# Optimization experiments

Hardware: AMD Instinct MI355X
Metric: run time of the kernel (lower is better)

The kernel has to match this reference:

```python
import jax, jax.numpy as jnp
import numpy as np

ATTN_SIZE = 64
ENC_SIZE = 512
HIDDEN_SIZE = 512
L, B = 2048, 64


def setup_inputs() -> dict:
    key = jax.random.key(0)
    k1, k2, k3, k4, k5, k6 = jax.random.split(key, 6)
    enc_outputs = jax.random.normal(k1, (L, B, ENC_SIZE), dtype=jnp.float32)
    lens = jax.random.randint(k2, (B,), 1, L + 1, dtype=jnp.int32)
    hidden_states = jax.random.normal(k3, (B, HIDDEN_SIZE), dtype=jnp.float32)
    # Xavier-normal params as in reset_params()
    W_enc = jax.random.normal(k4, (ENC_SIZE, ATTN_SIZE), dtype=jnp.float32) * np.sqrt(2.0 / (ENC_SIZE + ATTN_SIZE))
    W_hidden = jax.random.normal(k5, (HIDDEN_SIZE, ATTN_SIZE), dtype=jnp.float32) * np.sqrt(2.0 / (HIDDEN_SIZE + ATTN_SIZE))
    b_attn = jnp.zeros((ATTN_SIZE,), dtype=jnp.float32)
    v = jax.random.normal(k6, (ATTN_SIZE,), dtype=jnp.float32)
    return {"enc_outputs": enc_outputs, "lens": lens, "hidden_states": hidden_states,
            "W_enc": W_enc, "b_attn": b_attn, "W_hidden": W_hidden, "v": v}


def reference(enc_outputs, lens, hidden_states, W_enc, b_attn, W_hidden, v):
    l = enc_outputs.shape[0]
    # parts: (l, b, attn_size) — projection of encoder outputs
    parts = jnp.einsum('lbd,da->lba', enc_outputs, W_enc) + b_attn
    # additive (Bahdanau) score: tanh(parts + h @ W_hidden) . v -> (l, b)
    hid = hidden_states @ W_hidden  # (b, attn_size)
    scores = jnp.sum(jnp.tanh(parts + hid[None, :, :]) * v, axis=2)
    # faithful mask: 1.0 at valid positions, -inf at padding (original adds 1, a
    # constant shift that softmax cancels, but we reproduce the exact math)
    valid = jnp.arange(l, dtype=lens.dtype)[:, None] < lens[None, :]  # (l, b)
    mask = jnp.where(valid, jnp.float32(1.0), -jnp.inf)
    w = jax.nn.softmax(scores + mask, axis=0)  # softmax over sequence dim
    # weighted sum over sequence: (b, d)
    return jnp.einsum('lb,lbd->bd', w, enc_outputs)
```

## Files before the change

### kernel.cpp

```cpp
#include <hip/hip_runtime.h>
#include <hip/hip_bf16.h>
#include <math.h>

#define L_DIM 2048
#define B_DIM 64
#define D_DIM 512
#define A_DIM 64

#define SUB_L 16
#define CHUNK_L 64
#define N_SUB (CHUNK_L / SUB_L)
#define N_CHUNK (L_DIM / CHUNK_L)
#define EPAD 520

typedef __attribute__((ext_vector_type(8))) short bf16x8;
typedef __attribute__((ext_vector_type(4))) float f32x4;

__device__ __forceinline__ void split_bf16(float x, short& hi, short& lo) {
    __hip_bfloat16 h = __float2bfloat16(x);
    float hf = __bfloat162float(h);
    __hip_bfloat16 l = __float2bfloat16(x - hf);
    hi = *reinterpret_cast<short*>(&h);
    lo = *reinterpret_cast<short*>(&l);
}

__device__ __forceinline__ void split_pair(float x, float y,
                                           unsigned& hi2, unsigned& lo2) {
    unsigned ux = __float_as_uint(x), uy = __float_as_uint(y);
    hi2 = __builtin_amdgcn_perm(uy, ux, 0x07060302u);
    float rx = x - __uint_as_float(ux & 0xFFFF0000u);
    float ry = y - __uint_as_float(uy & 0xFFFF0000u);
    lo2 = __builtin_amdgcn_perm(__float_as_uint(ry), __float_as_uint(rx),
                                0x07060302u);
}

__device__ __forceinline__ float bf_hi_lo(short h, short l) {
    unsigned uh = ((unsigned)(unsigned short)h) << 16;
    unsigned ul = ((unsigned)(unsigned short)l) << 16;
    return __uint_as_float(uh) + __uint_as_float(ul);
}

__device__ __forceinline__ float fast_tanh(float x) {
    float e = __expf(2.0f * x);
    return 1.0f - 2.0f / (e + 1.0f);
}

__device__ __forceinline__ void lds_barrier() {
    asm volatile("s_waitcnt lgkmcnt(0)" ::: "memory");
    __builtin_amdgcn_s_barrier();
}

__global__ __launch_bounds__(256) void setup_kernel(
    const float* __restrict__ hidden, const float* __restrict__ Wh,
    const float* __restrict__ battn, const float* __restrict__ We,
    float* __restrict__ hb, short* __restrict__ wt_hi,
    short* __restrict__ wt_lo) {
    __shared__ float part[4][A_DIM];
    if (blockIdx.x < 64) {
        const int b = blockIdx.x;
        const int a = threadIdx.x & 63;
        const int sl = threadIdx.x >> 6;
        const float* hrow = hidden + b * D_DIM + sl * 128;
        const float* wcol = Wh + (size_t)sl * 128 * A_DIM + a;
        float acc = 0.f;
#pragma unroll 8
        for (int d = 0; d < 128; ++d) acc += hrow[d] * wcol[(size_t)d * A_DIM];
        part[sl][a] = acc;
        __syncthreads();
        if (sl == 0)
            hb[b * A_DIM + a] =
                battn[a] + part[0][a] + part[1][a] + part[2][a] + part[3][a];
    } else {
        const int base = (blockIdx.x - 64) * 1024 + threadIdx.x * 4;
#pragma unroll
        for (int t = 0; t < 4; ++t) {
            const int i = base + t;
            const int a = i & 63;
            const int d = i >> 6;
            short h, l;
            split_bf16(We[i], h, l);
            wt_hi[a * D_DIM + d] = h;
            wt_lo[a * D_DIM + d] = l;
        }
    }
}

__global__ __launch_bounds__(256, 2) void fused_kernel(
    const float* __restrict__ enc, const short* __restrict__ wt_hi,
    const short* __restrict__ wt_lo, const float* __restrict__ hb,
    const float* __restrict__ v, const int* __restrict__ lens,
    float* __restrict__ Om, float* __restrict__ mz) {
    const int c = blockIdx.x;
    const int b = blockIdx.y;
    const int tid = threadIdx.x;
    const int wave = tid >> 6;
    const int lane = tid & 63;
    const int quad = lane >> 4;
    const int l15 = lane & 15;
    const int po = tid & 127;
    const int par = tid >> 7;

    __shared__ short Ehi[2][SUB_L][EPAD];
    __shared__ short Elo[2][SUB_L][EPAD];
    __shared__ float sred[SUB_L][4];
    __shared__ float ored[D_DIM];

    const int len_b = lens[b];
    const int a_col = wave * 16 + l15;
    const float hb0 = hb[b * A_DIM + a_col];
    const float v0 = v[a_col];

    const short* bh = wt_hi + (size_t)a_col * D_DIM + quad * 8;
    const short* bl = wt_lo + (size_t)a_col * D_DIM + quad * 8;
    bf16x8 Bh[16], Bl[16];
#pragma unroll
    for (int s = 0; s < 16; ++s) {
        Bh[s] = *(const bf16x8*)(bh + s * 32);
        Bl[s] = *(const bf16x8*)(bl + s * 32);
    }

    float4 Oacc = {0.f, 0.f, 0.f, 0.f};
    float mA = -INFINITY, ZA = 0.f;

    const float* encb = enc + (size_t)c * CHUNK_L * B_DIM * D_DIM +
                        (size_t)b * D_DIM + po * 4;
    const size_t ROWSTRIDE = (size_t)B_DIM * D_DIM;

    float4 buf[8];
#pragma unroll
    for (int j = 0; j < 8; ++j)
        buf[j] = *(const float4*)(encb + (size_t)(2 * j + par) * ROWSTRIDE);

#pragma unroll 2
    for (int sub = 0; sub < N_SUB; ++sub) {
        const int cb = sub & 1;

#pragma unroll
        for (int j = 0; j < 8; ++j) {
            const int li = 2 * j + par;
            uint2 h2, l2;
            split_pair(buf[j].x, buf[j].y, h2.x, l2.x);
            split_pair(buf[j].z, buf[j].w, h2.y, l2.y);
            *(uint2*)&Ehi[cb][li][po * 4] = h2;
            *(uint2*)&Elo[cb][li][po * 4] = l2;
        }
        lds_barrier();

        if (sub + 1 < N_SUB) {
            const float* p = encb + (size_t)(sub + 1) * SUB_L * ROWSTRIDE;
#pragma unroll
            for (int j = 0; j < 8; ++j)
                buf[j] = *(const float4*)(p + (size_t)(2 * j + par) * ROWSTRIDE);
        }

        f32x4 a0 = {0.f, 0.f, 0.f, 0.f};
        f32x4 a1 = {0.f, 0.f, 0.f, 0.f};
        f32x4 a2 = {0.f, 0.f, 0.f, 0.f};
#pragma unroll
        for (int s = 0; s < 16; ++s) {
            const int k = s * 32;
            const bf16x8 Ah = *(const bf16x8*)&Ehi[cb][l15][k + quad * 8];
            const bf16x8 Al = *(const bf16x8*)&Elo[cb][l15][k + quad * 8];
            a0 = __builtin_amdgcn_mfma_f32_16x16x32_bf16(Ah, Bh[s], a0, 0, 0, 0);
            a1 = __builtin_amdgcn_mfma_f32_16x16x32_bf16(Ah, Bl[s], a1, 0, 0, 0);
            a2 = __builtin_amdgcn_mfma_f32_16x16x32_bf16(Al, Bh[s], a2, 0, 0, 0);
        }

#pragma unroll
        for (int r = 0; r < 4; ++r) {
            float t = fast_tanh(a0[r] + a1[r] + a2[r] + hb0) * v0;
            t += __shfl_xor(t, 1);
            t += __shfl_xor(t, 2);
            t += __shfl_xor(t, 4);
            t += __shfl_xor(t, 8);
            if (l15 == 0) sred[quad * 4 + r][wave] = t;
        }
        lds_barrier();

        float s = sred[l15][0] + sred[l15][1] + sred[l15][2] + sred[l15][3];
        const int lg = c * CHUNK_L + sub * SUB_L + l15;
        s = (lg < len_b) ? (s + 1.0f) : -INFINITY;
        float m = s;
        m = fmaxf(m, __shfl_xor(m, 1));
        m = fmaxf(m, __shfl_xor(m, 2));
        m = fmaxf(m, __shfl_xor(m, 4));
        m = fmaxf(m, __shfl_xor(m, 8));
        const float w = (m == -INFINITY) ? 0.f : __expf(s - m);
        float z = w;
        z += __shfl_xor(z, 1);
        z += __shfl_xor(z, 2);
        z += __shfl_xor(z, 4);
        z += __shfl_xor(z, 8);

        const float mN = fmaxf(mA, m);
        const float cA = (mA == -INFINITY) ? 0.f : __expf(mA - mN);
        const float cS = (m == -INFINITY) ? 0.f : __expf(m - mN);
        Oacc.x *= cA; Oacc.y *= cA; Oacc.z *= cA; Oacc.w *= cA;
#pragma unroll
        for (int j = 0; j < 8; ++j) {
            const int li = 2 * j + par;
            const float wgt = cS * __shfl(w, li);
            const short4 h4 = *(const short4*)&Ehi[cb][li][po * 4];
            const short4 l4 = *(const short4*)&Elo[cb][li][po * 4];
            Oacc.x += wgt * bf_hi_lo(h4.x, l4.x);
            Oacc.y += wgt * bf_hi_lo(h4.y, l4.y);
            Oacc.z += wgt * bf_hi_lo(h4.z, l4.z);
            Oacc.w += wgt * bf_hi_lo(h4.w, l4.w);
        }
        ZA = cA * ZA + cS * z;
        mA = mN;
    }

    if (par == 0) *(float4*)&ored[po * 4] = Oacc;
    __syncthreads();
    if (par == 1) {
        const float4 o0 = *(const float4*)&ored[po * 4];
        float4 r;
        r.x = o0.x + Oacc.x;
        r.y = o0.y + Oacc.y;
        r.z = o0.z + Oacc.z;
        r.w = o0.w + Oacc.w;
        *(float4*)(Om + ((size_t)b * N_CHUNK + c) * D_DIM + po * 4) = r;
    }
    if (tid == 0) {
        mz[((size_t)b * N_CHUNK + c) * 2 + 0] = mA;
        mz[((size_t)b * N_CHUNK + c) * 2 + 1] = ZA;
    }
}

__global__ __launch_bounds__(256) void combine_kernel(
    const float* __restrict__ Om, const float* __restrict__ mz,
    float* __restrict__ out) {
    const int b = blockIdx.x;
    const int tid = threadIdx.x;
    __shared__ float coef[N_CHUNK];
    __shared__ float sinv;

    if (tid < 32) {
        const float m = mz[((size_t)b * N_CHUNK + tid) * 2 + 0];
        const float Z = mz[((size_t)b * N_CHUNK + tid) * 2 + 1];
        float mm = m;
        mm = fmaxf(mm, __shfl_xor(mm, 1));
        mm = fmaxf(mm, __shfl_xor(mm, 2));
        mm = fmaxf(mm, __shfl_xor(mm, 4));
        mm = fmaxf(mm, __shfl_xor(mm, 8));
        mm = fmaxf(mm, __shfl_xor(mm, 16));
        const float cc = (m == -INFINITY) ? 0.f : __expf(m - mm);
        coef[tid] = cc;
        float s = cc * Z;
        s += __shfl_xor(s, 1);
        s += __shfl_xor(s, 2);
        s += __shfl_xor(s, 4);
        s += __shfl_xor(s, 8);
        s += __shfl_xor(s, 16);
        if (tid == 0) sinv = 1.0f / s;
    }
    __syncthreads();

    const float* base = Om + (size_t)b * N_CHUNK * D_DIM + tid * 2;
    float ox = 0.f, oy = 0.f;
#pragma unroll 8
    for (int cc = 0; cc < N_CHUNK; ++cc) {
        const float2 x = *(const float2*)(base + cc * D_DIM);
        ox += coef[cc] * x.x;
        oy += coef[cc] * x.y;
    }
    const float s = sinv;
    *(float2*)(out + (size_t)b * D_DIM + tid * 2) = make_float2(ox * s, oy * s);
}

extern "C" void kernel_launch(void* const* d_in, const int* in_sizes, int n_in,
                              void* d_out, int out_size, void* d_ws, size_t ws_size,
                              hipStream_t stream) {
    const float* enc    = (const float*)d_in[0];
    const int*   lens   = (const int*)d_in[1];
    const float* hidden = (const float*)d_in[2];
    const float* We     = (const float*)d_in[3];
    const float* battn  = (const float*)d_in[4];
    const float* Wh     = (const float*)d_in[5];
    const float* v      = (const float*)d_in[6];
    float* out = (float*)d_out;

    char* w8 = (char*)d_ws;
    float* hb    = (float*)(w8 + 0);
    short* wt_hi = (short*)(w8 + 16 * 1024);
    short* wt_lo = (short*)(w8 + 80 * 1024);
    float* mz    = (float*)(w8 + 144 * 1024);
    float* Om    = (float*)(w8 + 160 * 1024);

    setup_kernel<<<96, 256, 0, stream>>>(hidden, Wh, battn, We, hb, wt_hi, wt_lo);
    fused_kernel<<<dim3(N_CHUNK, B_DIM), 256, 0, stream>>>(
        enc, wt_hi, wt_lo, hb, v, lens, Om, mz);
    combine_kernel<<<B_DIM, 256, 0, stream>>>(Om, mz, out);
}
```

Baseline: 419.1 us.

## Single-buffer LDS, transpose MFMA operands, and simplify score reduction for higher occupancy

Drops the double-buffered E tiles to a single buffer and adds a trailing barrier so the LDS footprint shrinks, then raises launch bounds to allow three blocks per CU. Swaps MFMA operand order so each lane holds four attention columns of one row. The tanh·v reduction then needs only two cross-lane shuffles instead of sixteen. Every thread now recomputes the 16-row max and sum from shared memory, which removes the shuffle-based broadcast of weights. The risks are register spills under the tighter occupancy bound and the extra barrier per sub-tile.

Result: slower. 522.2 us (+24.6%).

```diff
diff --git a/kernel.cpp b/kernel.cpp
--- a/kernel.cpp
+++ b/kernel.cpp
@@ -85,7 +85,7 @@
     }
 }
 
-__global__ __launch_bounds__(256, 2) void fused_kernel(
+__global__ __launch_bounds__(256, 3) void fused_kernel(
     const float* __restrict__ enc, const short* __restrict__ wt_hi,
     const short* __restrict__ wt_lo, const float* __restrict__ hb,
     const float* __restrict__ v, const int* __restrict__ lens,
@@ -100,15 +100,15 @@
     const int po = tid & 127;
     const int par = tid >> 7;
 
-    __shared__ short Ehi[2][SUB_L][EPAD];
-    __shared__ short Elo[2][SUB_L][EPAD];
-    __shared__ float sred[SUB_L][4];
+    __shared__ short Ehi[SUB_L][EPAD];
+    __shared__ short Elo[SUB_L][EPAD];
+    __shared__ __align__(16) float sred[SUB_L][4];
     __shared__ float ored[D_DIM];
 
     const int len_b = lens[b];
     const int a_col = wave * 16 + l15;
-    const float hb0 = hb[b * A_DIM + a_col];
-    const float v0 = v[a_col];
+    const float4 hb4 = *(const float4*)(hb + b * A_DIM + wave * 16 + quad * 4);
+    const float4 v4  = *(const float4*)(v + wave * 16 + quad * 4);
 
     const short* bh = wt_hi + (size_t)a_col * D_DIM + quad * 8;
     const short* bl = wt_lo + (size_t)a_col * D_DIM + quad * 8;
@@ -131,18 +131,16 @@
     for (int j = 0; j < 8; ++j)
         buf[j] = *(const float4*)(encb + (size_t)(2 * j + par) * ROWSTRIDE);
 
-#pragma unroll 2
+#pragma unroll 1
     for (int sub = 0; sub < N_SUB; ++sub) {
-        const int cb = sub & 1;
-
 #pragma unroll
         for (int j = 0; j < 8; ++j) {
             const int li = 2 * j + par;
             uint2 h2, l2;
             split_pair(buf[j].x, buf[j].y, h2.x, l2.x);
             split_pair(buf[j].z, buf[j].w, h2.y, l2.y);
-            *(uint2*)&Ehi[cb][li][po * 4] = h2;
-            *(uint2*)&Elo[cb][li][po * 4] = l2;
+            *(uint2*)&Ehi[li][po * 4] = h2;
+            *(uint2*)&Elo[li][po * 4] = l2;
         }
         lds_barrier();
 
@@ -159,38 +157,40 @@
 #pragma unroll
         for (int s = 0; s < 16; ++s) {
             const int k = s * 32;
-            const bf16x8 Ah = *(const bf16x8*)&Ehi[cb][l15][k + quad * 8];
-            const bf16x8 Al = *(const bf16x8*)&Elo[cb][l15][k + quad * 8];
-            a0 = __builtin_amdgcn_mfma_f32_16x16x32_bf16(Ah, Bh[s], a0, 0, 0, 0);
-            a1 = __builtin_amdgcn_mfma_f32_16x16x32_bf16(Ah, Bl[s], a1, 0, 0, 0);
-            a2 = __builtin_amdgcn_mfma_f32_16x16x32_bf16(Al, Bh[s], a2, 0, 0, 0);
-        }
-
-#pragma unroll
-        for (int r = 0; r < 4; ++r) {
-            float t = fast_tanh(a0[r] + a1[r] + a2[r] + hb0) * v0;
-            t += __shfl_xor(t, 1);
-            t += __shfl_xor(t, 2);
-            t += __shfl_xor(t, 4);
-            t += __shfl_xor(t, 8);
-            if (l15 == 0) sred[quad * 4 + r][wave] = t;
-        }
+            const bf16x8 Ah = *(const bf16x8*)&Ehi[l15][k + quad * 8];
+            const bf16x8 Al = *(const bf16x8*)&Elo[l15][k + quad * 8];
+            a0 = __builtin_amdgcn_mfma_f32_16x16x32_bf16(Bh[s], Ah, a0, 0, 0, 0);
+            a1 = __builtin_amdgcn_mfma_f32_16x16x32_bf16(Bl[s], Ah, a1, 0, 0, 0);
+            a2 = __builtin_amdgcn_mfma_f32_16x16x32_bf16(Bh[s], Al, a2, 0, 0, 0);
+        }
+
+        float t = 0.f;
+#pragma unroll
+        for (int r = 0; r < 4; ++r)
+            t += fast_tanh(a0[r] + a1[r] + a2[r] + hb4[r]) * v4[r];
+        t += __shfl_xor(t, 16);
+        t += __shfl_xor(t, 32);
+        if (lane < 16) sred[lane][wave] = t;
         lds_barrier();
 
-        float s = sred[l15][0] + sred[l15][1] + sred[l15][2] + sred[l15][3];
-        const int lg = c * CHUNK_L + sub * SUB_L + l15;
-        s = (lg < len_b) ? (s + 1.0f) : -INFINITY;
-        float m = s;
-        m = fmaxf(m, __shfl_xor(m, 1));
-        m = fmaxf(m, __shfl_xor(m, 2));
-        m = fmaxf(m, __shfl_xor(m, 4));
-        m = fmaxf(m, __shfl_xor(m, 8));
-        const float w = (m == -INFINITY) ? 0.f : __expf(s - m);
-        float z = w;
-        z += __shfl_xor(z, 1);
-        z += __shfl_xor(z, 2);
-        z += __shfl_xor(z, 4);
-        z += __shfl_xor(z, 8);
+        const int lgbase = c * CHUNK_L + sub * SUB_L;
+        float sarr[SUB_L];
+        float m = -INFINITY;
+#pragma unroll
+        for (int r = 0; r < SUB_L; ++r) {
+            const float4 q = *(const float4*)&sred[r][0];
+            float s = q.x + q.y + q.z + q.w + 1.0f;
+            s = (lgbase + r < len_b) ? s : -INFINITY;
+            sarr[r] = s;
+            m = fmaxf(m, s);
+        }
+        float z = 0.f;
+#pragma unroll
+        for (int r = 0; r < SUB_L; ++r) {
+            const float w = (sarr[r] == -INFINITY) ? 0.f : __expf(sarr[r] - m);
+            sarr[r] = w;
+            z += w;
+        }
 
         const float mN = fmaxf(mA, m);
         const float cA = (mA == -INFINITY) ? 0.f : __expf(mA - mN);
@@ -199,9 +199,10 @@
 #pragma unroll
         for (int j = 0; j < 8; ++j) {
             const int li = 2 * j + par;
-            const float wgt = cS * __shfl(w, li);
-            const short4 h4 = *(const short4*)&Ehi[cb][li][po * 4];
-            const short4 l4 = *(const short4*)&Elo[cb][li][po * 4];
+            const float wsel = par ? sarr[2 * j + 1] : sarr[2 * j];
+            const float wgt = cS * wsel;
+            const short4 h4 = *(const short4*)&Ehi[li][po * 4];
+            const short4 l4 = *(const short4*)&Elo[li][po * 4];
             Oacc.x += wgt * bf_hi_lo(h4.x, l4.x);
             Oacc.y += wgt * bf_hi_lo(h4.y, l4.y);
             Oacc.z += wgt * bf_hi_lo(h4.z, l4.z);
@@ -209,6 +210,7 @@
         }
         ZA = cA * ZA + cS * z;
         mA = mN;
+        lds_barrier();
     }
 
     if (par == 0) *(float4*)&ored[po * 4] = Oacc;
```
